# Optimization experiments

Hardware: AMD Instinct MI355X
Metric: run time of the kernel (lower is better)

Reference implementation:

```python
import jax, jax.numpy as jnp
import numpy as np

TOP_K = 2  # num_experts_per_tok


def setup_inputs() -> dict:
    key = jax.random.key(0)
    ks = jax.random.split(key, 5)
    B, S, D, M, E = 4, 2048, 2048, 2048, 8
    x = jax.random.normal(ks[0], (B, S, D), dtype=jnp.float32)
    gate_kernel = jax.random.normal(ks[1], (D, E), dtype=jnp.float32) / np.sqrt(D)
    wi_0 = jax.random.normal(ks[2], (E, D, M), dtype=jnp.float32) / np.sqrt(D)
    wi_1 = jax.random.normal(ks[3], (E, D, M), dtype=jnp.float32) / np.sqrt(D)
    wo = jax.random.normal(ks[4], (E, M, D), dtype=jnp.float32) / np.sqrt(M)
    return {"x": x, "gate_kernel": gate_kernel, "wi_0": wi_0, "wi_1": wi_1, "wo": wo}


def reference(x, gate_kernel, wi_0, wi_1, wo):
    E = gate_kernel.shape[-1]
    # Gate logits: (B, S, E)
    gate_logits = jnp.einsum("bsd,de->bse", x, gate_kernel)
    # Top-k routing, then softmax over the selected experts' logits
    top_k_weights, top_k_indices = jax.lax.top_k(gate_logits, TOP_K)
    top_k_weights = jax.nn.softmax(top_k_weights.astype(jnp.float32), axis=-1).astype(x.dtype)
    # Dense combine weights per expert: (B, S, E)
    combine_w = jnp.sum(
        jax.nn.one_hot(top_k_indices, E, dtype=x.dtype) * top_k_weights[..., None], axis=-2
    )
    # Grouped GEMM (dense-masked form, as in MaxText dense_matmul path)
    h0 = jnp.einsum("bsd,edm->bsem", x, wi_0)  # (B, S, E, M)
    h1 = jnp.einsum("bsd,edm->bsem", x, wi_1)
    h = jax.nn.silu(h0) * h1 * combine_w[..., None]
    out = jnp.einsum("bsem,emd->bsd", h, wo)  # (B, S, D)
    return out
```

## Files before the change

kernel.cpp:

```cpp
#include <hip/hip_runtime.h>
#include <hip/hip_bf16.h>
#include <stdint.h>

#define TT   8192
#define DD   2048
#define MM   2048
#define NE   8

typedef float f32x4 __attribute__((ext_vector_type(4)));
typedef short s16x8 __attribute__((ext_vector_type(8)));
typedef unsigned int u32;
typedef unsigned long long u64;

static __device__ __forceinline__ short f2bf(float f) {
  __hip_bfloat16 h = __float2bfloat16(f);
  short s;
  __builtin_memcpy(&s, &h, 2);
  return s;
}
static __device__ __forceinline__ float bf2f(short s) {
  u32 u = ((u32)(unsigned short)s) << 16;
  float f;
  __builtin_memcpy(&f, &u, 4);
  return f;
}

static __device__ __forceinline__ void gload_lds16(const short* g, short* lds) {
  __builtin_amdgcn_global_load_lds(
      (const __attribute__((address_space(1))) u32*)g,
      (__attribute__((address_space(3))) u32*)lds, 16, 0, 0);
}

#define GCVT01  (16 * 32 * 32)

__global__ __launch_bounds__(256) void gate_fused(
    const float* __restrict__ x, const float* __restrict__ gk,
    int* __restrict__ counts, int* __restrict__ tkidx, float* __restrict__ tkw,
    short* __restrict__ xbf,
    const float* __restrict__ wi0, const float* __restrict__ wi1,
    short* __restrict__ o0, short* __restrict__ o1) {
  __shared__ short tile[64][65];
  __shared__ float red[4][NE];

  const int bid = blockIdx.x;
  if (bid >= TT) {
    const int idx = bid - TT;
    const int wz = idx >> 10;
    const float* in  = (wz < 8) ? wi0 : wi1;
    short* out       = (wz < 8) ? o0 : o1;
    const int ex = wz & 7;
    const int rem = idx & 1023;
    const int r0 = (rem >> 5) * 64;
    const int c0 = (rem & 31) * 64;
    const float* src = in + (size_t)ex * DD * MM;
    short* dst = out + (size_t)ex * DD * MM;
    const int t = threadIdx.x;
    const int rr = t >> 4, cc = (t & 15) * 4;
    #pragma unroll
    for (int i = 0; i < 4; i++) {
      int row = rr + i * 16;
      f32x4 v = *(const f32x4*)(src + (size_t)(r0 + row) * MM + c0 + cc);
      tile[cc + 0][row] = f2bf(v[0]);
      tile[cc + 1][row] = f2bf(v[1]);
      tile[cc + 2][row] = f2bf(v[2]);
      tile[cc + 3][row] = f2bf(v[3]);
    }
    __syncthreads();
    const int orow = t >> 2, c8 = (t & 3) * 16;
    s16x8 v0, v1;
    #pragma unroll
    for (int i = 0; i < 8; i++) { v0[i] = tile[orow][c8 + i]; v1[i] = tile[orow][c8 + 8 + i]; }
    short* dp = dst + (size_t)(c0 + orow) * DD + r0 + c8;
    *(s16x8*)(dp) = v0;
    *(s16x8*)(dp + 8) = v1;
    return;
  }

  const int t = bid;
  const float* xr = x + (size_t)t * DD;
  const int d0 = threadIdx.x * 8;
  f32x4 a = *(const f32x4*)(xr + d0);
  f32x4 b = *(const f32x4*)(xr + d0 + 4);
  s16x8 v;
  v[0]=f2bf(a[0]); v[1]=f2bf(a[1]); v[2]=f2bf(a[2]); v[3]=f2bf(a[3]);
  v[4]=f2bf(b[0]); v[5]=f2bf(b[1]); v[6]=f2bf(b[2]); v[7]=f2bf(b[3]);
  *(s16x8*)(xbf + (size_t)t * DD + d0) = v;

  float acc[NE];
  #pragma unroll
  for (int e = 0; e < NE; e++) acc[e] = 0.f;
  #pragma unroll
  for (int j = 0; j < 8; j++) {
    float xv = (j < 4) ? a[j] : b[j - 4];
    const float* g = gk + (size_t)(d0 + j) * NE;
    #pragma unroll
    for (int e = 0; e < NE; e++) acc[e] += xv * g[e];
  }
  #pragma unroll
  for (int e = 0; e < NE; e++) {
    #pragma unroll
    for (int off = 32; off >= 1; off >>= 1)
      acc[e] += __shfl_xor(acc[e], off, 64);
  }
  int wid = threadIdx.x >> 6;
  int lane = threadIdx.x & 63;
  if (lane == 0) {
    #pragma unroll
    for (int e = 0; e < NE; e++) red[wid][e] = acc[e];
  }
  __syncthreads();
  if (threadIdx.x == 0) {
    float l[NE];
    #pragma unroll
    for (int e = 0; e < NE; e++) l[e] = red[0][e] + red[1][e] + red[2][e] + red[3][e];
    int i1 = 0; float v1 = l[0];
    #pragma unroll
    for (int e = 1; e < NE; e++) if (l[e] > v1) { v1 = l[e]; i1 = e; }
    int i2 = -1; float v2 = -1e30f;
    #pragma unroll
    for (int e = 0; e < NE; e++) if (e != i1 && l[e] > v2) { v2 = l[e]; i2 = e; }
    float p = __expf(v2 - v1);
    float inv = 1.f / (1.f + p);
    tkidx[t*2]   = i1; tkidx[t*2+1] = i2;
    tkw[t*2]     = inv; tkw[t*2+1]  = p * inv;
    atomicAdd(&counts[i1], 1);
    atomicAdd(&counts[i2], 1);
  }
}

__global__ __launch_bounds__(256) void scatter_kernel(const int* __restrict__ counts,
    int* __restrict__ offsets, const int* __restrict__ tkidx,
    const float* __restrict__ tkw, int* __restrict__ ltok, float* __restrict__ lwt,
    int* __restrict__ slots) {
  const int e = blockIdx.x;
  const int tid = threadIdx.x;
  const int wid = tid >> 6, lane = tid & 63;
  __shared__ int base_s;
  __shared__ int wsum[4];
  if (tid == 0) {
    int s = 0;
    #pragma unroll
    for (int i = 0; i < NE; i++) {
      if (e == 0) offsets[i] = s;
      if (i < e) s += counts[i];
      else if (e == 0) s += counts[i];
    }
    if (e == 0) offsets[NE] = s;
    int bs = 0;
    for (int i = 0; i < e; i++) bs += counts[i];
    base_s = bs;
  }
  __syncthreads();
  int base = base_s;
  for (int it = 0; it < (TT * 2) / 256; it++) {
    int i = it * 256 + tid;
    bool m = (tkidx[i] == e);
    u64 b = __ballot(m);
    if (lane == 0) wsum[wid] = __popcll(b);
    __syncthreads();
    int pre = 0;
    #pragma unroll
    for (int w = 0; w < 4; w++) if (w < wid) pre += wsum[w];
    int tot = wsum[0] + wsum[1] + wsum[2] + wsum[3];
    int rank = __popcll(b & ((lane == 0) ? 0ull : ((1ull << lane) - 1ull)));
    if (m) {
      int dst = base + pre + rank;
      ltok[dst] = i >> 1;
      lwt[dst]  = tkw[i];
      slots[i]  = dst;
    }
    __syncthreads();
    base += tot;
  }
}

__global__ __launch_bounds__(256) void combine_kernel(const short* __restrict__ comb,
    const int* __restrict__ slots, float* __restrict__ out) {
  const int t = blockIdx.x;
  const int s0 = slots[2 * t], s1 = slots[2 * t + 1];
  const int idx = threadIdx.x;
  s16x8 a = *(const s16x8*)(comb + (size_t)s0 * DD + idx * 8);
  s16x8 b = *(const s16x8*)(comb + (size_t)s1 * DD + idx * 8);
  f32x4 o0, o1;
  #pragma unroll
  for (int j = 0; j < 4; j++) {
    o0[j] = bf2f(a[j]) + bf2f(b[j]);
    o1[j] = bf2f(a[4 + j]) + bf2f(b[4 + j]);
  }
  float* po = out + (size_t)t * DD + idx * 8;
  *(f32x4*)(po) = o0;
  *(f32x4*)(po + 4) = o1;
}

__device__ __forceinline__ void find_seg(const int* __restrict__ offsets, int tile, int bm,
                                         int& e, int& row0, int& rows, int& seg) {
  e = -1; row0 = 0; rows = 0; seg = 0;
  int accT = 0, prev = offsets[0];
  #pragma unroll
  for (int i = 0; i < NE; i++) {
    int nxt = offsets[i+1];
    int cnt = nxt - prev;
    int nt = (cnt + bm - 1) / bm;
    if (e < 0 && tile < accT + nt) { e = i; row0 = (tile - accT) * bm; rows = cnt; seg = prev; }
    accT += nt; prev = nxt;
  }
}

__device__ __forceinline__ void xcd_map(int ypx, int& tile, int& nyi) {
  const int bid = blockIdx.y * gridDim.x + blockIdx.x;
  const int xcd = bid & 7;
  const int i = bid >> 3;
  tile = i / ypx;
  nyi  = xcd * ypx + (i % ypx);
}

#define G1TILES 136
#define G1GRID  (G1TILES * 16)
#define GOGRID  (8 * 32 * 32)

__global__ __launch_bounds__(256, 2) void gemm1_fused(
    const short* __restrict__ xbf,
    const short* __restrict__ w0t, const short* __restrict__ w1t,
    const int* __restrict__ offsets,
    const int* __restrict__ ltok, const float* __restrict__ lwt,
    short* __restrict__ hbuf,
    const float* __restrict__ wo, short* __restrict__ wot) {
  __shared__ short As[128 * 64];
  __shared__ short B0s[128 * 64];
  __shared__ short B1s[128 * 64];
  __shared__ float w_s[128];

  const int bid = blockIdx.x;
  if (bid >= G1GRID) {
    short (*tile)[65] = (short(*)[65])As;
    const int idx = bid - G1GRID;
    const int ex = idx >> 10;
    const int rem = idx & 1023;
    const int r0 = (rem >> 5) * 64;
    const int c0 = (rem & 31) * 64;
    const float* src = wo + (size_t)ex * DD * MM;
    short* dst = wot + (size_t)ex * DD * MM;
    const int t = threadIdx.x;
    const int rr = t >> 4, cc = (t & 15) * 4;
    #pragma unroll
    for (int i = 0; i < 4; i++) {
      int row = rr + i * 16;
      f32x4 v = *(const f32x4*)(src + (size_t)(r0 + row) * MM + c0 + cc);
      tile[cc + 0][row] = f2bf(v[0]);
      tile[cc + 1][row] = f2bf(v[1]);
      tile[cc + 2][row] = f2bf(v[2]);
      tile[cc + 3][row] = f2bf(v[3]);
    }
    __syncthreads();
    const int orow = t >> 2, c8 = (t & 3) * 16;
    s16x8 v0, v1;
    #pragma unroll
    for (int i = 0; i < 8; i++) { v0[i] = tile[orow][c8 + i]; v1[i] = tile[orow][c8 + 8 + i]; }
    short* dp = dst + (size_t)(c0 + orow) * DD + r0 + c8;
    *(s16x8*)(dp) = v0;
    *(s16x8*)(dp + 8) = v1;
    return;
  }

  const int xcd = bid & 7;
  const int bi = bid >> 3;
  const int tile = bi >> 1;
  const int nyi = xcd * 2 + (bi & 1);
  const int n0 = nyi * 128;
  int e, row0, rows, seg;
  find_seg(offsets, tile, 128, e, row0, rows, seg);
  if (e < 0) return;

  const int tid = threadIdx.x;
  const int lane = tid & 63, wid = tid >> 6;
  if (tid < 128) {
    int gr = row0 + tid;
    w_s[tid] = (gr < rows) ? lwt[seg + gr] : 0.f;
  }

  const int swz = ((lane & 7) ^ (lane >> 3)) * 8;
  const short* abase[4];
  const short* b0base[4];
  const short* b1base[4];
  #pragma unroll
  for (int c = 0; c < 4; c++) {
    int chunk = wid * 4 + c;
    int r = chunk * 8 + (lane >> 3);
    int gr = row0 + r; if (gr >= rows) gr = rows - 1;
    int tok = ltok[seg + gr];
    abase[c]  = xbf + (size_t)tok * DD + swz;
    int n = n0 + r;
    b0base[c] = w0t + ((size_t)e * MM + n) * DD + swz;
    b1base[c] = w1t + ((size_t)e * MM + n) * DD + swz;
  }

  const int wr = wid >> 1, wc = wid & 1;
  const int lr = lane & 15;
  const int kq = (lane >> 4) * 8;

  f32x4 acc0[4][4], acc1[4][4];
  #pragma unroll
  for (int i = 0; i < 4; i++)
    #pragma unroll
    for (int j = 0; j < 4; j++) { acc0[i][j] = 0.f; acc1[i][j] = 0.f; }

  for (int k0 = 0; k0 < DD; k0 += 64) {
    #pragma unroll
    for (int c = 0; c < 4; c++) {
      int chunk = wid * 4 + c;
      gload_lds16(abase[c]  + k0, As  + chunk * 512);
      gload_lds16(b0base[c] + k0, B0s + chunk * 512);
      gload_lds16(b1base[c] + k0, B1s + chunk * 512);
    }
    __syncthreads();

    #pragma unroll
    for (int ks = 0; ks < 2; ks++) {
      s16x8 a[4], b0[4], b1[4];
      #pragma unroll
      for (int mi = 0; mi < 4; mi++) {
        int row = wr * 64 + mi * 16 + lr;
        int koff = (ks * 32 + kq) ^ ((row & 7) * 8);
        a[mi] = *(const s16x8*)&As[row * 64 + koff];
      }
      #pragma unroll
      for (int ni = 0; ni < 4; ni++) {
        int row = wc * 64 + ni * 16 + lr;
        int koff = (ks * 32 + kq) ^ ((row & 7) * 8);
        b0[ni] = *(const s16x8*)&B0s[row * 64 + koff];
        b1[ni] = *(const s16x8*)&B1s[row * 64 + koff];
      }
      #pragma unroll
      for (int mi = 0; mi < 4; mi++)
        #pragma unroll
        for (int ni = 0; ni < 4; ni++) {
          acc0[mi][ni] = __builtin_amdgcn_mfma_f32_16x16x32_bf16(a[mi], b0[ni], acc0[mi][ni], 0, 0, 0);
          acc1[mi][ni] = __builtin_amdgcn_mfma_f32_16x16x32_bf16(a[mi], b1[ni], acc1[mi][ni], 0, 0, 0);
        }
    }
    __syncthreads();
  }

  const int lq = lane >> 4;
  #pragma unroll
  for (int mi = 0; mi < 4; mi++) {
    #pragma unroll
    for (int jj = 0; jj < 4; jj++) {
      int r = wr * 64 + mi * 16 + lq * 4 + jj;
      int gr = row0 + r;
      if (gr < rows) {
        float wgt = w_s[r];
        size_t hrow = (size_t)(seg + gr) * MM + n0;
        #pragma unroll
        for (int ni = 0; ni < 4; ni++) {
          int c = wc * 64 + ni * 16 + lr;
          float g = acc0[mi][ni][jj];
          float u = acc1[mi][ni][jj];
          float act = g / (1.f + __expf(-g));
          hbuf[hrow + c] = f2bf(act * u * wgt);
        }
      }
    }
  }
}

__global__ __launch_bounds__(256, 2) void gemm2_fast(
    const short* __restrict__ hbuf,
    const short* __restrict__ wot,
    const int* __restrict__ offsets,
    short* __restrict__ comb) {
  __shared__ short As[128 * 64];
  __shared__ short B0s[128 * 64];
  __shared__ short B1s[128 * 64];

  int tile, nyi;
  xcd_map(1, tile, nyi);
  const int n0 = nyi * 256;
  int e, row0, rows, seg;
  find_seg(offsets, tile, 128, e, row0, rows, seg);
  if (e < 0) return;

  const int tid = threadIdx.x;
  const int lane = tid & 63, wid = tid >> 6;

  const int swz = ((lane & 7) ^ (lane >> 3)) * 8;
  const short* abase[4];
  const short* b0base[4];
  const short* b1base[4];
  #pragma unroll
  for (int c = 0; c < 4; c++) {
    int chunk = wid * 4 + c;
    int r = chunk * 8 + (lane >> 3);
    int gr = row0 + r; if (gr >= rows) gr = rows - 1;
    abase[c] = hbuf + (size_t)(seg + gr) * MM + swz;
    b0base[c] = wot + ((size_t)e * DD + n0 + r) * MM + swz;
    b1base[c] = wot + ((size_t)e * DD + n0 + 128 + r) * MM + swz;
  }

  const int wr = wid >> 1, wc = wid & 1;
  const int lr = lane & 15;
  const int kq = (lane >> 4) * 8;

  f32x4 acc0[4][4], acc1[4][4];
  #pragma unroll
  for (int i = 0; i < 4; i++)
    #pragma unroll
    for (int j = 0; j < 4; j++) { acc0[i][j] = 0.f; acc1[i][j] = 0.f; }

  for (int k0 = 0; k0 < MM; k0 += 64) {
    #pragma unroll
    for (int c = 0; c < 4; c++) {
      int chunk = wid * 4 + c;
      gload_lds16(abase[c]  + k0, As  + chunk * 512);
      gload_lds16(b0base[c] + k0, B0s + chunk * 512);
      gload_lds16(b1base[c] + k0, B1s + chunk * 512);
    }
    __syncthreads();

    #pragma unroll
    for (int ks = 0; ks < 2; ks++) {
      s16x8 a[4], b0[4], b1[4];
      #pragma unroll
      for (int mi = 0; mi < 4; mi++) {
        int row = wr * 64 + mi * 16 + lr;
        int koff = (ks * 32 + kq) ^ ((row & 7) * 8);
        a[mi] = *(const s16x8*)&As[row * 64 + koff];
      }
      #pragma unroll
      for (int ni = 0; ni < 4; ni++) {
        int row = wc * 64 + ni * 16 + lr;
        int koff = (ks * 32 + kq) ^ ((row & 7) * 8);
        b0[ni] = *(const s16x8*)&B0s[row * 64 + koff];
        b1[ni] = *(const s16x8*)&B1s[row * 64 + koff];
      }
      #pragma unroll
      for (int mi = 0; mi < 4; mi++)
        #pragma unroll
        for (int ni = 0; ni < 4; ni++) {
          acc0[mi][ni] = __builtin_amdgcn_mfma_f32_16x16x32_bf16(a[mi], b0[ni], acc0[mi][ni], 0, 0, 0);
          acc1[mi][ni] = __builtin_amdgcn_mfma_f32_16x16x32_bf16(a[mi], b1[ni], acc1[mi][ni], 0, 0, 0);
        }
    }
    __syncthreads();
  }

  const int lq = lane >> 4;
  #pragma unroll
  for (int mi = 0; mi < 4; mi++) {
    #pragma unroll
    for (int jj = 0; jj < 4; jj++) {
      int r = wr * 64 + mi * 16 + lq * 4 + jj;
      int gr = row0 + r;
      if (gr < rows) {
        size_t orow = (size_t)(seg + gr) * DD + n0;
        #pragma unroll
        for (int ni = 0; ni < 4; ni++) {
          int c = wc * 64 + ni * 16 + lr;
          comb[orow + c] = f2bf(acc0[mi][ni][jj]);
          comb[orow + 128 + c] = f2bf(acc1[mi][ni][jj]);
        }
      }
    }
  }
}

extern "C" void kernel_launch(void* const* d_in, const int* in_sizes, int n_in,
                              void* d_out, int out_size, void* d_ws, size_t ws_size,
                              hipStream_t stream) {
  const float* x   = (const float*)d_in[0];
  const float* gk  = (const float*)d_in[1];
  const float* wi0 = (const float*)d_in[2];
  const float* wi1 = (const float*)d_in[3];
  const float* wo  = (const float*)d_in[4];
  float* out = (float*)d_out;

  char* w = (char*)d_ws;
  int*   counts  = (int*)(w);
  int*   offsets = (int*)(w + 256);
  int*   tkidx   = (int*)(w + 1024);
  float* tkw     = (float*)(w + 1024 + 65536);
  int*   ltok    = (int*)(w + 1024 + 2*65536);
  float* lwt     = (float*)(w + 1024 + 3*65536);
  int*   slots   = (int*)(w + 1024 + 4*65536);
  short* xbf  = (short*)(w + 524288);
  short* hbuf = xbf + (size_t)TT * DD;
  short* w0t  = hbuf + (size_t)2 * TT * MM;
  short* w1t  = w0t + (size_t)NE * DD * MM;
  short* wot  = w1t + (size_t)NE * DD * MM;
  short* comb = w0t;

  hipMemsetAsync(counts, 0, 64, stream);

  gate_fused<<<TT + GCVT01, 256, 0, stream>>>(x, gk, counts, tkidx, tkw, xbf,
                                              wi0, wi1, w0t, w1t);
  scatter_kernel<<<NE, 256, 0, stream>>>(counts, offsets, tkidx, tkw, ltok, lwt, slots);

  gemm1_fused<<<G1GRID + GOGRID, 256, 0, stream>>>(xbf, w0t, w1t, offsets, ltok, lwt,
                                                   hbuf, wo, wot);
  gemm2_fast<<<dim3(G1TILES, DD/256), 256, 0, stream>>>(hbuf, wot, offsets, comb);
  combine_kernel<<<TT, 256, 0, stream>>>(comb, slots, out);
}
```

Before: 839.2 us.

## Split gemm2 K dimension in halves across blocks, reduce in combine kernel

The down-projection GEMM is split into two K-halves, each handled by a separate block that writes bf16 partial outputs to its own buffer, doubling the grid. The combine kernel now sums both partials for each of the two token slots. This raises the number of blocks in gemm2, which was only 136x8 tiles, to improve CU occupancy and tail behaviour. In exchange it adds extra partial-output traffic and reads in combine, plus one more bf16 rounding of the partial sums.

```diff
diff --git a/kernel.cpp b/kernel.cpp
--- a/kernel.cpp
+++ b/kernel.cpp
@@ -174,18 +174,21 @@
   }
 }
 
-__global__ __launch_bounds__(256) void combine_kernel(const short* __restrict__ comb,
-    const int* __restrict__ slots, float* __restrict__ out) {
+__global__ __launch_bounds__(256) void combine_kernel(const short* __restrict__ c0,
+    const short* __restrict__ c1, const int* __restrict__ slots,
+    float* __restrict__ out) {
   const int t = blockIdx.x;
   const int s0 = slots[2 * t], s1 = slots[2 * t + 1];
   const int idx = threadIdx.x;
-  s16x8 a = *(const s16x8*)(comb + (size_t)s0 * DD + idx * 8);
-  s16x8 b = *(const s16x8*)(comb + (size_t)s1 * DD + idx * 8);
+  s16x8 a0 = *(const s16x8*)(c0 + (size_t)s0 * DD + idx * 8);
+  s16x8 a1 = *(const s16x8*)(c1 + (size_t)s0 * DD + idx * 8);
+  s16x8 b0 = *(const s16x8*)(c0 + (size_t)s1 * DD + idx * 8);
+  s16x8 b1 = *(const s16x8*)(c1 + (size_t)s1 * DD + idx * 8);
   f32x4 o0, o1;
   #pragma unroll
   for (int j = 0; j < 4; j++) {
-    o0[j] = bf2f(a[j]) + bf2f(b[j]);
-    o1[j] = bf2f(a[4 + j]) + bf2f(b[4 + j]);
+    o0[j] = (bf2f(a0[j]) + bf2f(a1[j])) + (bf2f(b0[j]) + bf2f(b1[j]));
+    o1[j] = (bf2f(a0[4+j]) + bf2f(a1[4+j])) + (bf2f(b0[4+j]) + bf2f(b1[4+j]));
   }
   float* po = out + (size_t)t * DD + idx * 8;
   *(f32x4*)(po) = o0;
@@ -204,14 +207,6 @@
     if (e < 0 && tile < accT + nt) { e = i; row0 = (tile - accT) * bm; rows = cnt; seg = prev; }
     accT += nt; prev = nxt;
   }
-}
-
-__device__ __forceinline__ void xcd_map(int ypx, int& tile, int& nyi) {
-  const int bid = blockIdx.y * gridDim.x + blockIdx.x;
-  const int xcd = bid & 7;
-  const int i = bid >> 3;
-  tile = i / ypx;
-  nyi  = xcd * ypx + (i % ypx);
 }
 
 #define G1TILES 136
@@ -368,14 +363,19 @@
     const short* __restrict__ hbuf,
     const short* __restrict__ wot,
     const int* __restrict__ offsets,
-    short* __restrict__ comb) {
+    short* __restrict__ comb0, short* __restrict__ comb1) {
   __shared__ short As[128 * 64];
   __shared__ short B0s[128 * 64];
   __shared__ short B1s[128 * 64];
 
-  int tile, nyi;
-  xcd_map(1, tile, nyi);
+  const int bid = blockIdx.y * gridDim.x + blockIdx.x;
+  const int xcd = bid & 7;
+  const int i = bid >> 3;
+  const int kh = i & 1;
+  const int tile = i >> 1;
+  const int nyi = xcd;
   const int n0 = nyi * 256;
+  const int kbase = kh * (MM / 2);
   int e, row0, rows, seg;
   find_seg(offsets, tile, 128, e, row0, rows, seg);
   if (e < 0) return;
@@ -392,9 +392,9 @@
     int chunk = wid * 4 + c;
     int r = chunk * 8 + (lane >> 3);
     int gr = row0 + r; if (gr >= rows) gr = rows - 1;
-    abase[c] = hbuf + (size_t)(seg + gr) * MM + swz;
-    b0base[c] = wot + ((size_t)e * DD + n0 + r) * MM + swz;
-    b1base[c] = wot + ((size_t)e * DD + n0 + 128 + r) * MM + swz;
+    abase[c] = hbuf + (size_t)(seg + gr) * MM + kbase + swz;
+    b0base[c] = wot + ((size_t)e * DD + n0 + r) * MM + kbase + swz;
+    b1base[c] = wot + ((size_t)e * DD + n0 + 128 + r) * MM + kbase + swz;
   }
 
   const int wr = wid >> 1, wc = wid & 1;
@@ -403,11 +403,11 @@
 
   f32x4 acc0[4][4], acc1[4][4];
   #pragma unroll
-  for (int i = 0; i < 4; i++)
-    #pragma unroll
-    for (int j = 0; j < 4; j++) { acc0[i][j] = 0.f; acc1[i][j] = 0.f; }
-
-  for (int k0 = 0; k0 < MM; k0 += 64) {
+  for (int i2 = 0; i2 < 4; i2++)
+    #pragma unroll
+    for (int j = 0; j < 4; j++) { acc0[i2][j] = 0.f; acc1[i2][j] = 0.f; }
+
+  for (int k0 = 0; k0 < MM / 2; k0 += 64) {
     #pragma unroll
     for (int c = 0; c < 4; c++) {
       int chunk = wid * 4 + c;
@@ -444,6 +444,7 @@
     __syncthreads();
   }
 
+  short* comb = kh ? comb1 : comb0;
   const int lq = lane >> 4;
   #pragma unroll
   for (int mi = 0; mi < 4; mi++) {
@@ -487,7 +488,8 @@
   short* w0t  = hbuf + (size_t)2 * TT * MM;
   short* w1t  = w0t + (size_t)NE * DD * MM;
   short* wot  = w1t + (size_t)NE * DD * MM;
-  short* comb = w0t;
+  short* comb0 = w0t;
+  short* comb1 = w1t;
 
   hipMemsetAsync(counts, 0, 64, stream);
 
@@ -497,6 +499,6 @@
 
   gemm1_fused<<<G1GRID + GOGRID, 256, 0, stream>>>(xbf, w0t, w1t, offsets, ltok, lwt,
                                                    hbuf, wo, wot);
-  gemm2_fast<<<dim3(G1TILES, DD/256), 256, 0, stream>>>(hbuf, wot, offsets, comb);
-  combine_kernel<<<TT, 256, 0, stream>>>(comb, slots, out);
-}
+  gemm2_fast<<<dim3(G1TILES, 16), 256, 0, stream>>>(hbuf, wot, offsets, comb0, comb1);
+  combine_kernel<<<TT, 256, 0, stream>>>(comb0, comb1, slots, out);
+}
```

Measured after the change: 845.2 us. Within noise of the previous version (+0.7%).
